# Performance work log

Hardware: AMD Instinct MI355X
Metric: run time of the kernel (lower is better)

## Reference

```python
import jax, jax.numpy as jnp
import numpy as np

GRID = 24          # sqrt(576)
MM = 1024          # mm_hidden_size
HID = 4096         # hidden_size
HEADS = 8          # mm_hidden_size // 128
NQ = GRID * GRID   # 576 queries / tokens
BATCH = 16
K = 2              # top-k == num_experts == 2


def _sincos_1d(d, pos):
    omega = np.arange(d // 2, dtype=np.float32) / (d / 2.0)
    omega = 1.0 / 10000 ** omega
    out = np.einsum('m,d->md', pos.reshape(-1).astype(np.float32), omega)
    return np.concatenate([np.sin(out), np.cos(out)], axis=1)


def _sincos_2d(d, g):
    gw, gh = np.meshgrid(np.arange(g, dtype=np.float32), np.arange(g, dtype=np.float32))
    return np.concatenate([_sincos_1d(d // 2, gh), _sincos_1d(d // 2, gw)], axis=1)


def layer_norm(x, g, b, eps=1e-5):
    mu = x.mean(-1, keepdims=True)
    var = ((x - mu) ** 2).mean(-1, keepdims=True)
    return (x - mu) * jax.lax.rsqrt(var + eps) * g + b


def mha(q, k, v, Wi, bi, Wo, bo, H):
    # q,k,v: [N, S, D]; Wi: [3D, D]; torch nn.MultiheadAttention semantics
    N, S, D = q.shape
    dh = D // H
    Wq, Wk, Wv = Wi[:D], Wi[D:2 * D], Wi[2 * D:]
    bq, bk, bv = bi[:D], bi[D:2 * D], bi[2 * D:]
    qp = (q @ Wq.T + bq).reshape(N, S, H, dh)
    kp = (k @ Wk.T + bk).reshape(N, -1, H, dh)
    vp = (v @ Wv.T + bv).reshape(N, -1, H, dh)
    scale = jnp.asarray(1.0 / np.sqrt(dh), q.dtype)
    scores = jnp.einsum('bqhd,bkhd->bhqk', qp, kp) * scale
    attn = jax.nn.softmax(scores, axis=-1)
    out = jnp.einsum('bhqk,bkhd->bqhd', attn, vp).reshape(N, S, D)
    return out @ Wo.T + bo


def _gating(xf, w_gate, w_noise, noise):
    # noisy top-k gating, training mode, k == num_experts == 2
    clean = xf @ w_gate                               # [B, 2]
    std = jax.nn.softplus(xf @ w_noise) + 0.01
    logits = jax.nn.softmax(clean + noise * std, axis=1)
    top_vals, top_idx = jax.lax.top_k(logits, K)      # min(k+1, n) == 2
    gates_k = top_vals / (top_vals.sum(1, keepdims=True) + 1e-6)
    rows = jnp.arange(xf.shape[0])[:, None]
    return jnp.zeros_like(logits).at[rows, top_idx].set(gates_k)


def setup_inputs() -> dict:
    key = jax.random.key(0)
    ks = jax.random.split(key, 10)
    s = 0.02
    f32 = jnp.float32
    return dict(
        x=jax.random.normal(ks[0], (BATCH, NQ, MM), f32),
        noise=jax.random.normal(ks[1], (BATCH * NQ, 2), f32),
        W1=jax.random.normal(ks[2], (HID, MM), f32) * s,
        b1=jnp.zeros((HID,), f32),
        W2=jax.random.normal(ks[3], (HID, HID), f32) * s,
        b2=jnp.zeros((HID,), f32),
        query=jax.random.normal(ks[4], (NQ, MM), f32) * s,
        pos_embed=jnp.asarray(_sincos_2d(MM, GRID), f32),
        ln_q_g=jnp.ones((MM,), f32), ln_q_b=jnp.zeros((MM,), f32),
        ln_kv_g=jnp.ones((MM,), f32), ln_kv_b=jnp.zeros((MM,), f32),
        in_proj_w=jax.random.normal(ks[5], (3 * MM, MM), f32) * s,
        in_proj_b=jnp.zeros((3 * MM,), f32),
        out_w=jax.random.normal(ks[6], (MM, MM), f32) * s,
        out_b=jnp.zeros((MM,), f32),
        w_gate=jax.random.normal(ks[7], (MM, 2), f32) * s,
        w_noise=jax.random.normal(ks[8], (MM, 2), f32) * s,
    )


def reference(x, noise, W1, b1, W2, b2, query, pos_embed, ln_q_g, ln_q_b,
              ln_kv_g, ln_kv_b, in_proj_w, in_proj_b, out_w, out_b,
              w_gate, w_noise):
    N, C, D = x.shape

    def projection(t):  # Linear -> GELU(exact) -> Linear
        h = jax.nn.gelu(t @ W1.T + b1, approximate=False)
        return h @ W2.T + b2

    # --- Resampler expert (kv_proj/ln_post/proj are identity here) ---
    kv = layer_norm(x, ln_kv_g, ln_kv_b)                    # [N, 576, D]
    q = layer_norm(query, ln_q_g, ln_q_b) + pos_embed       # [576, D]
    q = jnp.broadcast_to(q, (N, C, D))
    attn_out = mha(q, kv + pos_embed, kv, in_proj_w, in_proj_b, out_w, out_b, HEADS)

    e0 = projection(x)          # expert 0: MLP projection
    e1 = projection(attn_out)   # expert 1: resampler then projection

    gates = _gating(x.reshape(N * C, D), w_gate, w_noise, noise).reshape(N, C, 2)
    # stack(...,-1) @ gates[...,None] squeezed == gated sum over experts
    return e0 * gates[..., 0:1] + e1 * gates[..., 1:2]
```

## Files before the change

kernel.cpp:

```cpp
#include <hip/hip_runtime.h>
#include <hip/hip_bf16.h>
#include <cstdint>
#include <cstddef>


typedef __bf16 bf16;
typedef __bf16 bf16x4 __attribute__((ext_vector_type(4)));
typedef __bf16 bf16x8 __attribute__((ext_vector_type(8)));
typedef float  f32x4  __attribute__((ext_vector_type(4)));

#define BATCH 16
#define NQ    576
#define MM    1024
#define HID   4096
#define HEADS 8
#define DH    128
#define ROWS  (BATCH*NQ)

typedef const unsigned int __attribute__((address_space(1)))* gas_ptr;
typedef unsigned int __attribute__((address_space(3)))* las_ptr;

__device__ __forceinline__ void async16(const bf16* g, bf16* l) {
  __builtin_amdgcn_global_load_lds((gas_ptr)g, (las_ptr)l, 16, 0, 0);
}

__global__ __launch_bounds__(256) void cvt_kernel(
    const float* __restrict__ s, bf16* __restrict__ d)
{
  const int i = (blockIdx.x * 256 + threadIdx.x) * 4;
  f32x4 v = *(const f32x4*)(s + i);
  bf16x4 o;
#pragma unroll
  for (int j = 0; j < 4; ++j) o[j] = (bf16)v[j];
  *(bf16x4*)(d + i) = o;
}

enum { MODE_BIAS = 0, MODE_GG = 1, MODE_GGACC = 2, MODE_GB = 3 };

template <int MODE, typename OutT>
__global__ __launch_bounds__(256) void gemm_bt(
    const bf16* __restrict__ A, const bf16* __restrict__ W,
    const float* __restrict__ bias, OutT* __restrict__ C,
    const float* __restrict__ gates, int M, int N, int K)
{
  __shared__ bf16 As[128 * 32];
  __shared__ bf16 Bs[128 * 32];

  const int tid  = threadIdx.x;
  const int lane = tid & 63;
  const int w    = tid >> 6;
  const int wm   = (w & 1) * 64;
  const int wn   = (w >> 1) * 64;
  const int l15  = lane & 15;
  const int quad = lane >> 4;
  const int m0   = blockIdx.y * 128;
  const int n0   = blockIdx.x * 128;

  f32x4 acc[4][4] = {};

  int ar0 = m0 + (tid >> 2);      if (ar0 > M - 1) ar0 = M - 1;
  int ar1 = m0 + 64 + (tid >> 2); if (ar1 > M - 1) ar1 = M - 1;
  const int kc = (tid & 3) * 8;
  const bf16* ap0 = A + (size_t)ar0 * K + kc;
  const bf16* ap1 = A + (size_t)ar1 * K + kc;
  const bf16* bp0 = W + (size_t)(n0 + (tid >> 2)) * K + kc;
  const bf16* bp1 = W + (size_t)(n0 + 64 + (tid >> 2)) * K + kc;
  bf16* lA0 = As + tid * 8;
  bf16* lA1 = As + 2048 + tid * 8;
  bf16* lB0 = Bs + tid * 8;
  bf16* lB1 = Bs + 2048 + tid * 8;

  const int ko = quad * 8;

  for (int kt = 0; kt < K; kt += 32) {
    async16(ap0 + kt, lA0);
    async16(ap1 + kt, lA1);
    async16(bp0 + kt, lB0);
    async16(bp1 + kt, lB1);
    __syncthreads();

    bf16x8 af[4], bfr[4];
#pragma unroll
    for (int i = 0; i < 4; ++i)
      af[i] = *(const bf16x8*)(As + (wm + i * 16 + l15) * 32 + ko);
#pragma unroll
    for (int i = 0; i < 4; ++i)
      bfr[i] = *(const bf16x8*)(Bs + (wn + i * 16 + l15) * 32 + ko);
#pragma unroll
    for (int mi = 0; mi < 4; ++mi)
#pragma unroll
      for (int ni = 0; ni < 4; ++ni)
        acc[mi][ni] = __builtin_amdgcn_mfma_f32_16x16x32_bf16(
            af[mi], bfr[ni], acc[mi][ni], 0, 0, 0);
    __syncthreads();
  }

#pragma unroll
  for (int ni = 0; ni < 4; ++ni) {
    const int col = n0 + wn + ni * 16 + l15;
    const float bv = bias[col];
#pragma unroll
    for (int mi = 0; mi < 4; ++mi) {
      const int rowb = m0 + wm + mi * 16 + quad * 4;
#pragma unroll
      for (int r = 0; r < 4; ++r) {
        const int gr = rowb + r;
        if (gr < M) {
          const size_t idx = (size_t)gr * N + col;
          if (MODE == MODE_GB) {
            C[idx] = (OutT)(acc[mi][ni][r] +
                            (gates[gr * 2] + gates[gr * 2 + 1]) * bv);
          } else {
            float v = acc[mi][ni][r] + bv;
            if (MODE == MODE_GG || MODE == MODE_GGACC)
              v = 0.5f * v * (1.0f + erff(v * 0.70710678118654752f));
            if (MODE == MODE_GG)
              C[idx] = (OutT)(v * gates[gr * 2]);
            else if (MODE == MODE_GGACC)
              C[idx] = (OutT)((float)C[idx] + v * gates[gr * 2 + 1]);
            else
              C[idx] = (OutT)v;
          }
        }
      }
    }
  }
}

__global__ __launch_bounds__(256) void attn_kernel(
    const bf16* __restrict__ qp, const bf16* __restrict__ kp,
    const bf16* __restrict__ vp, bf16* __restrict__ ctx)
{
  __shared__ bf16 Qs[64 * 128];
  __shared__ bf16 Ks[64 * 128];
  __shared__ bf16 Vt[128 * 64];
  __shared__ bf16 Ps[64 * 64];

  const int qt = blockIdx.x, b = blockIdx.y, h = blockIdx.z;
  const int tid = threadIdx.x, lane = tid & 63, w = tid >> 6;
  const int l15 = lane & 15, quad = lane >> 4;
  const int q0 = qt * 64;

#pragma unroll
  for (int i = 0; i < 4; ++i) {
    const int c = i * 256 + tid;
    const int row = c >> 4, col = (c & 15) * 8;
    *(bf16x8*)(Qs + row * 128 + col) =
        *(const bf16x8*)(qp + (size_t)(q0 + row) * MM + h * DH + col);
  }

  float m_r[4], l_r[4];
  f32x4 accO[8] = {};
#pragma unroll
  for (int r = 0; r < 4; ++r) { m_r[r] = -1e30f; l_r[r] = 0.f; }

  const float scale = 0.08838834764831843f;

  for (int kt = 0; kt < 9; ++kt) {
    __syncthreads();
    const int kbase = b * NQ + kt * 64;
#pragma unroll
    for (int i = 0; i < 4; ++i) {
      const int c = i * 256 + tid;
      const int row = c >> 4, col = (c & 15) * 8;
      *(bf16x8*)(Ks + row * 128 + col) =
          *(const bf16x8*)(kp + (size_t)(kbase + row) * MM + h * DH + col);
      bf16x8 vv = *(const bf16x8*)(vp + (size_t)(kbase + row) * MM + h * DH + col);
#pragma unroll
      for (int j = 0; j < 8; ++j) Vt[(col + j) * 64 + row] = vv[j];
    }
    __syncthreads();

    f32x4 sacc[4] = {};
#pragma unroll
    for (int kcq = 0; kcq < 4; ++kcq) {
      bf16x8 aq = *(const bf16x8*)(Qs + (w * 16 + l15) * 128 + kcq * 32 + quad * 8);
#pragma unroll
      for (int ni = 0; ni < 4; ++ni) {
        bf16x8 bk = *(const bf16x8*)(Ks + (ni * 16 + l15) * 128 + kcq * 32 + quad * 8);
        sacc[ni] = __builtin_amdgcn_mfma_f32_16x16x32_bf16(aq, bk, sacc[ni], 0, 0, 0);
      }
    }
#pragma unroll
    for (int ni = 0; ni < 4; ++ni)
#pragma unroll
      for (int r = 0; r < 4; ++r) sacc[ni][r] *= scale;

    float p[4][4];
#pragma unroll
    for (int r = 0; r < 4; ++r) {
      float mx = fmaxf(fmaxf(sacc[0][r], sacc[1][r]), fmaxf(sacc[2][r], sacc[3][r]));
#pragma unroll
      for (int off = 8; off >= 1; off >>= 1) mx = fmaxf(mx, __shfl_xor(mx, off, 64));
      const float mnew = fmaxf(m_r[r], mx);
      const float al = expf(m_r[r] - mnew);
      float rs = 0.f;
#pragma unroll
      for (int ni = 0; ni < 4; ++ni) { p[ni][r] = expf(sacc[ni][r] - mnew); rs += p[ni][r]; }
#pragma unroll
      for (int off = 8; off >= 1; off >>= 1) rs += __shfl_xor(rs, off, 64);
      l_r[r] = l_r[r] * al + rs;
      m_r[r] = mnew;
#pragma unroll
      for (int ni2 = 0; ni2 < 8; ++ni2) accO[ni2][r] *= al;
    }

#pragma unroll
    for (int ni = 0; ni < 4; ++ni)
#pragma unroll
      for (int r = 0; r < 4; ++r)
        Ps[(w * 16 + quad * 4 + r) * 64 + ni * 16 + l15] = (bf16)p[ni][r];

#pragma unroll
    for (int kc2 = 0; kc2 < 2; ++kc2) {
      bf16x8 ap = *(const bf16x8*)(Ps + (w * 16 + l15) * 64 + kc2 * 32 + quad * 8);
#pragma unroll
      for (int ni2 = 0; ni2 < 8; ++ni2) {
        bf16x8 bv = *(const bf16x8*)(Vt + (ni2 * 16 + l15) * 64 + kc2 * 32 + quad * 8);
        accO[ni2] = __builtin_amdgcn_mfma_f32_16x16x32_bf16(ap, bv, accO[ni2], 0, 0, 0);
      }
    }
  }

#pragma unroll
  for (int r = 0; r < 4; ++r) {
    const float inv = 1.0f / l_r[r];
    const int qrow = q0 + w * 16 + quad * 4 + r;
#pragma unroll
    for (int ni2 = 0; ni2 < 8; ++ni2)
      ctx[(size_t)(b * NQ + qrow) * MM + h * DH + ni2 * 16 + l15] =
          (bf16)(accO[ni2][r] * inv);
  }
}

__global__ __launch_bounds__(256) void lnx_kernel(
    const float* __restrict__ x, const float* __restrict__ g,
    const float* __restrict__ bta, const float* __restrict__ pos,
    const float* __restrict__ wg, const float* __restrict__ wn,
    const float* __restrict__ noise,
    bf16* __restrict__ kv, bf16* __restrict__ kin,
    bf16* __restrict__ x_bf, float* __restrict__ gates)
{
  const int row = blockIdx.x, tid = threadIdx.x;
  f32x4 xv = *(const f32x4*)(x + (size_t)row * MM + tid * 4);

  float s = 0.f, ss = 0.f, a0 = 0.f, a1 = 0.f, c0 = 0.f, c1 = 0.f;
#pragma unroll
  for (int j = 0; j < 4; ++j) {
    const int c = tid * 4 + j;
    s  += xv[j];
    ss += xv[j] * xv[j];
    a0 += xv[j] * wg[c * 2];
    a1 += xv[j] * wg[c * 2 + 1];
    c0 += xv[j] * wn[c * 2];
    c1 += xv[j] * wn[c * 2 + 1];
  }

  {
    bf16x4 o;
#pragma unroll
    for (int j = 0; j < 4; ++j) o[j] = (bf16)xv[j];
    *(bf16x4*)(x_bf + (size_t)row * MM + tid * 4) = o;
  }

#pragma unroll
  for (int off = 32; off >= 1; off >>= 1) {
    s  += __shfl_xor(s,  off, 64);  ss += __shfl_xor(ss, off, 64);
    a0 += __shfl_xor(a0, off, 64);  a1 += __shfl_xor(a1, off, 64);
    c0 += __shfl_xor(c0, off, 64);  c1 += __shfl_xor(c1, off, 64);
  }
  __shared__ float red[24];
  const int w = tid >> 6;
  if ((tid & 63) == 0) {
    red[w * 6]     = s;  red[w * 6 + 1] = ss;
    red[w * 6 + 2] = a0; red[w * 6 + 3] = a1;
    red[w * 6 + 4] = c0; red[w * 6 + 5] = c1;
  }
  __syncthreads();
  s  = red[0] + red[6]  + red[12] + red[18];
  ss = red[1] + red[7]  + red[13] + red[19];

  const float mu   = s * (1.0f / MM);
  const float rsig = rsqrtf(ss * (1.0f / MM) - mu * mu + 1e-5f);
  const int prow = row % NQ;
#pragma unroll
  for (int j = 0; j < 4; ++j) {
    const int c = tid * 4 + j;
    const float y = (xv[j] - mu) * rsig * g[c] + bta[c];
    kv[(size_t)row * MM + c]  = (bf16)y;
    kin[(size_t)row * MM + c] = (bf16)(y + pos[(size_t)prow * MM + c]);
  }

  if (tid == 0) {
    a0 = red[2] + red[8]  + red[14] + red[20];
    a1 = red[3] + red[9]  + red[15] + red[21];
    c0 = red[4] + red[10] + red[16] + red[22];
    c1 = red[5] + red[11] + red[17] + red[23];
    const float sp0 = fmaxf(c0, 0.f) + log1pf(expf(-fabsf(c0)));
    const float sp1 = fmaxf(c1, 0.f) + log1pf(expf(-fabsf(c1)));
    const float l0 = a0 + noise[row * 2]     * (sp0 + 0.01f);
    const float l1 = a1 + noise[row * 2 + 1] * (sp1 + 0.01f);
    const float mx = fmaxf(l0, l1);
    const float e0 = expf(l0 - mx), e1 = expf(l1 - mx);
    const float inv = 1.0f / (e0 + e1);
    const float p0 = e0 * inv, p1 = e1 * inv;
    const float den = 1.0f / (p0 + p1 + 1e-6f);
    gates[row * 2]     = p0 * den;
    gates[row * 2 + 1] = p1 * den;
  }
}

__global__ __launch_bounds__(256) void ln_q_kernel(
    const float* __restrict__ query, const float* __restrict__ g,
    const float* __restrict__ bta, const float* __restrict__ pos,
    bf16* __restrict__ qout)
{
  const int row = blockIdx.x, tid = threadIdx.x;
  f32x4 xv = *(const f32x4*)(query + (size_t)row * MM + tid * 4);
  float s = 0.f, ss = 0.f;
#pragma unroll
  for (int j = 0; j < 4; ++j) { s += xv[j]; ss += xv[j] * xv[j]; }
#pragma unroll
  for (int off = 32; off >= 1; off >>= 1) { s += __shfl_xor(s, off, 64); ss += __shfl_xor(ss, off, 64); }
  __shared__ float red[8];
  const int w = tid >> 6;
  if ((tid & 63) == 0) { red[w] = s; red[4 + w] = ss; }
  __syncthreads();
  s  = red[0] + red[1] + red[2] + red[3];
  ss = red[4] + red[5] + red[6] + red[7];
  const float mu = s * (1.0f / MM);
  const float rsig = rsqrtf(ss * (1.0f / MM) - mu * mu + 1e-5f);
#pragma unroll
  for (int j = 0; j < 4; ++j) {
    const int c = tid * 4 + j;
    const float y = (xv[j] - mu) * rsig * g[c] + bta[c] + pos[(size_t)row * MM + c];
    qout[(size_t)row * MM + c] = (bf16)y;
  }
}

extern "C" void kernel_launch(void* const* d_in, const int* in_sizes, int n_in,
                              void* d_out, int out_size, void* d_ws, size_t ws_size,
                              hipStream_t stream)
{
  const float* x       = (const float*)d_in[0];
  const float* noise   = (const float*)d_in[1];
  const float* W1      = (const float*)d_in[2];
  const float* b1      = (const float*)d_in[3];
  const float* W2      = (const float*)d_in[4];
  const float* b2      = (const float*)d_in[5];
  const float* query   = (const float*)d_in[6];
  const float* pos     = (const float*)d_in[7];
  const float* ln_q_g  = (const float*)d_in[8];
  const float* ln_q_b  = (const float*)d_in[9];
  const float* ln_kv_g = (const float*)d_in[10];
  const float* ln_kv_b = (const float*)d_in[11];
  const float* ipw     = (const float*)d_in[12];
  const float* ipb     = (const float*)d_in[13];
  const float* out_w   = (const float*)d_in[14];
  const float* out_b   = (const float*)d_in[15];
  const float* w_gate  = (const float*)d_in[16];
  const float* w_noise = (const float*)d_in[17];
  float* out = (float*)d_out;

  char* ws = (char*)d_ws;
  bf16*  kin   = (bf16*)(ws);
  bf16*  ctx   = kin;
  bf16*  kp    = (bf16*)(ws + 18874368);
  bf16*  vp    = (bf16*)(ws + 37748736);
  bf16*  qbuf  = (bf16*)(ws + 56623104);
  bf16*  qp    = (bf16*)(ws + 57802752);
  bf16*  ipwb  = (bf16*)(ws + 58982400);
  bf16*  outwb = (bf16*)(ws + 65273856);
  bf16*  h     = (bf16*)(ws);
  bf16*  x_bf  = (bf16*)(ws + 75497472);
  bf16*  W1b   = (bf16*)(ws + 94371840);
  bf16*  W2b   = (bf16*)(ws + 102760448);
  float* gates = (float*)(ws + 136314880);
  bf16*  kv       = (bf16*)d_out;
  bf16*  attn_out = (bf16*)((char*)d_out + 18874368);

  cvt_kernel<<<4096,  256, 0, stream>>>(W1, W1b);
  cvt_kernel<<<16384, 256, 0, stream>>>(W2, W2b);
  cvt_kernel<<<3072,  256, 0, stream>>>(ipw,   ipwb);
  cvt_kernel<<<1024,  256, 0, stream>>>(out_w, outwb);
  lnx_kernel<<<ROWS, 256, 0, stream>>>(x, ln_kv_g, ln_kv_b, pos,
                                       w_gate, w_noise, noise,
                                       kv, kin, x_bf, gates);
  ln_q_kernel<<<NQ, 256, 0, stream>>>(query, ln_q_g, ln_q_b, pos, qbuf);

  gemm_bt<MODE_BIAS, bf16><<<dim3(8, 5),  256, 0, stream>>>(qbuf, ipwb, ipb, qp, nullptr, NQ, MM, MM);
  gemm_bt<MODE_BIAS, bf16><<<dim3(8, 72), 256, 0, stream>>>(kin, ipwb + (size_t)MM * MM, ipb + MM, kp, nullptr, ROWS, MM, MM);
  gemm_bt<MODE_BIAS, bf16><<<dim3(8, 72), 256, 0, stream>>>(kv, ipwb + (size_t)2 * MM * MM, ipb + 2 * MM, vp, nullptr, ROWS, MM, MM);

  attn_kernel<<<dim3(9, BATCH, HEADS), 256, 0, stream>>>(qp, kp, vp, ctx);

  gemm_bt<MODE_BIAS, bf16><<<dim3(8, 72), 256, 0, stream>>>(ctx, outwb, out_b, attn_out, nullptr, ROWS, MM, MM);

  gemm_bt<MODE_GG,    bf16><<<dim3(32, 72), 256, 0, stream>>>(x_bf,     W1b, b1, h, gates, ROWS, HID, MM);
  gemm_bt<MODE_GGACC, bf16><<<dim3(32, 72), 256, 0, stream>>>(attn_out, W1b, b1, h, gates, ROWS, HID, MM);
  gemm_bt<MODE_GB,   float><<<dim3(32, 72), 256, 0, stream>>>(h,        W2b, b2, out, gates, ROWS, HID, HID);
}
```

Before: 1.400 ms.

## Double GEMM K-tile to 64 and XOR-swizzle LDS layout

Raises the GEMM K step from 32 to 64, which halves the number of barrier-separated load/compute iterations, and issues four async global-to-LDS loads per operand per tile. The LDS layout gets an XOR swizzle on the 16-byte chunk index so that fragment reads across lanes avoid bank conflicts. The cost is double the shared memory per block (32KB) and more in-flight loads, which may reduce occupancy. Each iteration still synchronises without any prefetch overlap.

```diff
diff --git a/kernel.cpp b/kernel.cpp
--- a/kernel.cpp
+++ b/kernel.cpp
@@ -43,8 +43,8 @@
     const float* __restrict__ bias, OutT* __restrict__ C,
     const float* __restrict__ gates, int M, int N, int K)
 {
-  __shared__ bf16 As[128 * 32];
-  __shared__ bf16 Bs[128 * 32];
+  __shared__ bf16 As[128 * 64];
+  __shared__ bf16 Bs[128 * 64];
 
   const int tid  = threadIdx.x;
   const int lane = tid & 63;
@@ -58,34 +58,50 @@
 
   f32x4 acc[4][4] = {};
 
-  int ar0 = m0 + (tid >> 2);      if (ar0 > M - 1) ar0 = M - 1;
-  int ar1 = m0 + 64 + (tid >> 2); if (ar1 > M - 1) ar1 = M - 1;
-  const int kc = (tid & 3) * 8;
-  const bf16* ap0 = A + (size_t)ar0 * K + kc;
-  const bf16* ap1 = A + (size_t)ar1 * K + kc;
-  const bf16* bp0 = W + (size_t)(n0 + (tid >> 2)) * K + kc;
-  const bf16* bp1 = W + (size_t)(n0 + 64 + (tid >> 2)) * K + kc;
-  bf16* lA0 = As + tid * 8;
-  bf16* lA1 = As + 2048 + tid * 8;
-  bf16* lB0 = Bs + tid * 8;
-  bf16* lB1 = Bs + 2048 + tid * 8;
-
-  const int ko = quad * 8;
-
-  for (int kt = 0; kt < K; kt += 32) {
-    async16(ap0 + kt, lA0);
-    async16(ap1 + kt, lA1);
-    async16(bp0 + kt, lB0);
-    async16(bp1 + kt, lB1);
+  const int srow0  = tid >> 3;
+  const int schunk = (tid & 7) ^ (srow0 & 7);
+  int arows[4], brows[4];
+#pragma unroll
+  for (int j = 0; j < 4; ++j) {
+    int r = m0 + j * 32 + srow0; if (r > M - 1) r = M - 1;
+    arows[j] = r;
+    brows[j] = n0 + j * 32 + srow0;
+  }
+  const int kc = schunk * 8;
+  bf16* lA = As + tid * 8;
+  bf16* lB = Bs + tid * 8;
+
+  const int axb  = (quad ^ (l15 & 7)) * 8;
+  const int axb1 = axb ^ 32;
+
+  for (int kt = 0; kt < K; kt += 64) {
+#pragma unroll
+    for (int j = 0; j < 4; ++j)
+      async16(A + (size_t)arows[j] * K + kt + kc, lA + j * 2048);
+#pragma unroll
+    for (int j = 0; j < 4; ++j)
+      async16(W + (size_t)brows[j] * K + kt + kc, lB + j * 2048);
     __syncthreads();
 
     bf16x8 af[4], bfr[4];
 #pragma unroll
     for (int i = 0; i < 4; ++i)
-      af[i] = *(const bf16x8*)(As + (wm + i * 16 + l15) * 32 + ko);
+      af[i] = *(const bf16x8*)(As + (wm + i * 16 + l15) * 64 + axb);
 #pragma unroll
     for (int i = 0; i < 4; ++i)
-      bfr[i] = *(const bf16x8*)(Bs + (wn + i * 16 + l15) * 32 + ko);
+      bfr[i] = *(const bf16x8*)(Bs + (wn + i * 16 + l15) * 64 + axb);
+#pragma unroll
+    for (int mi = 0; mi < 4; ++mi)
+#pragma unroll
+      for (int ni = 0; ni < 4; ++ni)
+        acc[mi][ni] = __builtin_amdgcn_mfma_f32_16x16x32_bf16(
+            af[mi], bfr[ni], acc[mi][ni], 0, 0, 0);
+#pragma unroll
+    for (int i = 0; i < 4; ++i)
+      af[i] = *(const bf16x8*)(As + (wm + i * 16 + l15) * 64 + axb1);
+#pragma unroll
+    for (int i = 0; i < 4; ++i)
+      bfr[i] = *(const bf16x8*)(Bs + (wn + i * 16 + l15) * 64 + axb1);
 #pragma unroll
     for (int mi = 0; mi < 4; ++mi)
 #pragma unroll
```

After: 1.335 ms. 4.7% less time.
